# Optimization experiments

Hardware: AMD Instinct MI355X
Metric: run time of the kernel (lower is better)

Reference implementation:

```python
import jax, jax.numpy as jnp
import numpy as np

N = 32768      # total atoms in batch
D_IN = 1024    # input feature dimension
H1 = 512       # encoder/decoder hidden width
LAT = 128      # latent dimension
D_OUT = 1024   # output dimension
E = 4          # number of unique element symbols (experts)


def _xavier(key, shape):
    # torch.nn.init.xavier_uniform_ on Linear weights
    fan_in, fan_out = shape[-2], shape[-1]
    limit = np.sqrt(6.0 / (fan_in + fan_out)).astype(np.float32)
    return jax.random.uniform(key, shape, jnp.float32, -limit, limit)


def setup_inputs() -> dict:
    key = jax.random.key(0)
    ks = jax.random.split(key, 8)
    X = jax.random.normal(ks[0], (N, D_IN), jnp.float32)
    sym_ids = jax.random.randint(ks[1], (N,), 0, E)
    # stacked per-symbol (expert) weights: topology 1024->512->128->512->1024
    We1 = _xavier(ks[2], (E, D_IN, H1));  be1 = jnp.zeros((E, H1), jnp.float32)
    We2 = _xavier(ks[3], (E, H1, LAT));   be2 = jnp.zeros((E, LAT), jnp.float32)
    Wd1 = _xavier(ks[4], (E, LAT, H1));   bd1 = jnp.zeros((E, H1), jnp.float32)
    Wd2 = _xavier(ks[5], (E, H1, D_OUT)); bd2 = jnp.zeros((E, D_OUT), jnp.float32)
    return {"X": X, "sym_ids": sym_ids,
            "We1": We1, "be1": be1, "We2": We2, "be2": be2,
            "Wd1": Wd1, "bd1": bd1, "Wd2": Wd2, "bd2": bd2}


def reference(X, sym_ids, We1, be1, We2, be2, Wd1, bd1, Wd2, bd2):
    # Dense MoE-style dispatch: compute every expert on the full batch (E is
    # tiny and fixed), then select each atom's own-symbol output. Same math as
    # the per-atom Python-loop routing in the original forward.
    def expert(e):
        h = jax.nn.relu(X @ We1[e] + be1[e])          # [N, H1]  encoder layer 1
        z = jax.nn.relu(h @ We2[e] + be2[e])          # [N, LAT] latent (encoder layer 2)
        d = jax.nn.relu(z @ Wd1[e] + bd1[e])          # [N, H1]  decoder layer 1
        return d @ Wd2[e] + bd2[e]                    # [N, D_OUT] final Linear, no activation

    outs = jnp.stack([expert(e) for e in range(E)])   # [E, N, D_OUT]
    # route: pick expert sym_ids[n] for atom n
    return jnp.take_along_axis(outs, sym_ids[None, :, None], axis=0)[0]
```

## Files before the change

### kernel.cpp

```cpp
#include <hip/hip_runtime.h>
#include <hip/hip_bf16.h>
#include <stdint.h>

typedef __bf16 bf16x8 __attribute__((ext_vector_type(8)));
typedef float  f32x4  __attribute__((ext_vector_type(4)));

#define NATOMS  32768
#define NEXP    4
#define MAXROWS (NATOMS + NEXP*256)
#define MB256   (MAXROWS/256)
#define MB128   (MAXROWS/128)
#define MGRP    ((MB256 + 7)/8)
#define XCONV   2048
#define SCAT    32

#define WS_HDR   0u
#define WS_PERM  1024u
#define WS_BC    136192u
#define WS_BB    138240u
#define WS_W1T   140288u
#define WS_W2T   (WS_W1T + 4194304u)
#define WS_W3T   (WS_W2T + 524288u)
#define WS_W4T   (WS_W3T + 524288u)
#define WS_H     (WS_W4T + 4194304u)
#define WS_D     WS_H
#define WS_XB    (WS_H + 34603008u)

__device__ __forceinline__ unsigned short f2bf(float f){
  union { float f; uint32_t u; } v; v.f = f;
  uint32_t r = v.u + 0x7fffu + ((v.u >> 16) & 1u);
  return (unsigned short)(r >> 16);
}
__device__ __forceinline__ uint32_t pk2(float a, float b){
  return (uint32_t)f2bf(a) | ((uint32_t)f2bf(b) << 16);
}
__device__ __forceinline__ void glds16(const void* g, void* l){
  __builtin_amdgcn_global_load_lds(
      (const __attribute__((address_space(1))) uint32_t*)g,
      (__attribute__((address_space(3))) uint32_t*)l, 16, 0, 0);
}

__global__ __launch_bounds__(256) void routeA(const int* __restrict__ sym,
                                              int* __restrict__ bc,
                                              int* __restrict__ perm){
  __shared__ int h[NEXP];
  const int t = threadIdx.x, b = blockIdx.x;
  if (t < NEXP) h[t] = 0;
  for (int i = b*256 + t; i < MAXROWS; i += 128*256) perm[i] = -1;
  __syncthreads();
  int s = sym[b*256 + t];
  atomicAdd(&h[s], 1);
  __syncthreads();
  if (t < NEXP) bc[b*NEXP + t] = h[t];
}

__global__ __launch_bounds__(64) void routeB(const int* __restrict__ bc,
                                             int* __restrict__ hdr,
                                             int* __restrict__ bb){
  __shared__ int tot[NEXP], pof[NEXP+1];
  const int t = threadIdx.x;
  if (t < NEXP){
    int s = 0;
    for (int i=0;i<128;++i) s += bc[i*NEXP + t];
    tot[t] = s;
  }
  __syncthreads();
  if (t == 0){
    int o = 0; pof[0] = 0;
    for (int e=0;e<NEXP;++e){ o += (tot[e]+255)&~255; pof[e+1]=o; }
    for (int e=0;e<=NEXP;++e) hdr[e]=pof[e];
  }
  __syncthreads();
  if (t < NEXP){
    int run = pof[t];
    for (int i=0;i<128;++i){ bb[i*NEXP + t] = run; run += bc[i*NEXP + t]; }
  }
}

template<int K, int NO>
__device__ __forceinline__ void wtile1024(const float* __restrict__ W,
                                          unsigned short* __restrict__ Bt,
                                          int b, unsigned short (*tile)[65]){
  const int nx = NO/64, ny = K/64;
  const int e = b / (nx*ny), rem = b % (nx*ny);
  const int k0 = (rem / nx) * 64;
  const int n0 = (rem % nx) * 64;
  const int t  = threadIdx.x;
  const int c  = t & 63;
  const float* Wb = W + ((size_t)e*K + k0)*NO + n0;
  #pragma unroll
  for (int i=0;i<4;++i){
    int r = (t>>6) + i*16;
    tile[r][c] = f2bf(Wb[(size_t)r*NO + c]);
  }
  __syncthreads();
  unsigned short* Bb = Bt + ((size_t)e*NO + n0)*K + k0;
  #pragma unroll
  for (int i=0;i<4;++i){
    int r = (t>>6) + i*16;
    Bb[(size_t)r*K + c] = tile[c][r];
  }
}

__global__ __launch_bounds__(1024) void prep_kernel(
    const int*   __restrict__ sym,  const int* __restrict__ bb,  int* __restrict__ perm,
    const float* __restrict__ X,    unsigned short* __restrict__ Xb,
    const float* __restrict__ We1, unsigned short* __restrict__ W1t,
    const float* __restrict__ We2, unsigned short* __restrict__ W2t,
    const float* __restrict__ Wd1, unsigned short* __restrict__ W3t,
    const float* __restrict__ Wd2, unsigned short* __restrict__ W4t)
{
  __shared__ unsigned short tile[64][65];
  __shared__ int wc[16][NEXP];

  int b = blockIdx.x;
  const int t = threadIdx.x;

  if (b < SCAT){
    const int lane = t & 63, w = t >> 6;
    const int a = b*1024 + t;
    const int s = sym[a];
    unsigned long long b0 = __ballot(s & 1);
    unsigned long long b1 = __ballot(s & 2);
    unsigned long long meq = ((s & 1) ? b0 : ~b0) & ((s & 2) ? b1 : ~b1);
    unsigned long long lt  = ((unsigned long long)1 << lane) - 1;
    const int lofs = __popcll(meq & lt);
    if (lane == 0){
      unsigned long long m00 = ~b0 & ~b1, m01 = b0 & ~b1, m10 = ~b0 & b1, m11 = b0 & b1;
      wc[w][0] = __popcll(m00); wc[w][1] = __popcll(m01);
      wc[w][2] = __popcll(m10); wc[w][3] = __popcll(m11);
    }
    __syncthreads();
    int wbase = 0;
    for (int i=0;i<w;++i) wbase += wc[i][s];
    const int rb = (t >> 8);
    int wbase_rb = 0;
    for (int i = rb*4; i < w; ++i) wbase_rb += wc[i][s];
    const int slot = bb[(b*4 + rb)*NEXP + s] + wbase_rb + lofs;
    perm[slot] = a;
    (void)wbase;
    return;
  }
  b -= SCAT;
  if (b < XCONV){
    size_t i = ((size_t)b*1024 + t) * 16;
    const float4* src = (const float4*)(X + i);
    float4 f0 = src[0], f1 = src[1], f2 = src[2], f3 = src[3];
    uint4 o0, o1;
    o0.x = pk2(f0.x,f0.y); o0.y = pk2(f0.z,f0.w);
    o0.z = pk2(f1.x,f1.y); o0.w = pk2(f1.z,f1.w);
    o1.x = pk2(f2.x,f2.y); o1.y = pk2(f2.z,f2.w);
    o1.z = pk2(f3.x,f3.y); o1.w = pk2(f3.z,f3.w);
    *(uint4*)&Xb[i]     = o0;
    *(uint4*)&Xb[i + 8] = o1;
    return;
  }
  b -= XCONV;
  if (b < 512){ wtile1024<1024, 512>(We1, W1t, b, tile); return; }
  b -= 512;
  if (b <  64){ wtile1024< 512, 128>(We2, W2t, b, tile); return; }
  b -= 64;
  if (b <  64){ wtile1024< 128, 512>(Wd1, W3t, b, tile); return; }
  b -= 64;
  wtile1024< 512,1024>(Wd2, W4t, b, tile);
}

template<int K, int NO, int NT, bool RELU, bool GATHER, bool FINAL>
__global__ __launch_bounds__(512, 4) void gemm_big(
    const unsigned short* __restrict__ A,
    const unsigned short* __restrict__ Bt,
    const float* __restrict__ bias,
    unsigned short* __restrict__ Cb,
    float* __restrict__ Cf,
    const int* __restrict__ hdr,
    const int* __restrict__ perm)
{
  __shared__ __align__(16) unsigned short smem[256*64 + 128*64];
  __shared__ int sperm[256];
  unsigned short* As = smem;
  unsigned short* Bs = smem + 256*64;

  const int b = blockIdx.x;
  const int grp = b / (8*NT), rem = b % (8*NT);
  const int rowblk = grp*8 + (rem & 7);
  const int row0 = rowblk * 256;
  if (row0 >= hdr[NEXP]) return;
  const int ntile = rem >> 3;
  const int e = (row0 >= hdr[1]) + (row0 >= hdr[2]) + (row0 >= hdr[3]);
  const int n0 = ntile * 128;

  const int t = threadIdx.x;
  const int lane = t & 63, wid = t >> 6;

  if constexpr (GATHER || FINAL){
    if (t < 256) sperm[t] = perm[row0 + t];
    __syncthreads();
  }

  const int l8 = lane >> 3;
  const int scoff = (((lane & 7) ^ l8) << 3);

  const unsigned short* asrc[4];
  #pragma unroll
  for (int i=0;i<4;++i){
    const int r = wid*32 + i*8 + l8;
    long grow;
    if constexpr (GATHER){
      int a = sperm[r];
      grow = (a < 0) ? 0 : a;
    } else {
      grow = row0 + r;
    }
    asrc[i] = A + (size_t)grow*K + scoff;
  }
  const unsigned short* bsrc[2];
  #pragma unroll
  for (int i=0;i<2;++i)
    bsrc[i] = Bt + ((size_t)e*NO + n0 + wid*16 + i*8 + l8)*K + scoff;

  const int lr   = lane & 15;
  const int sgrp = lane >> 4;
  const int wr   = (wid >> 1) * 64;
  const int wc   = (wid & 1) * 64;

  f32x4 acc[4][4];
  const f32x4 z4 = {0.f,0.f,0.f,0.f};
  #pragma unroll
  for (int mi=0;mi<4;++mi)
    #pragma unroll
    for (int ni=0;ni<4;++ni) acc[mi][ni] = z4;

  #pragma unroll 1
  for (int kt = 0; kt < K/64; ++kt){
    __syncthreads();
    #pragma unroll
    for (int i=0;i<4;++i)
      glds16(asrc[i] + kt*64, As + (wid*4+i)*512);
    #pragma unroll
    for (int i=0;i<2;++i)
      glds16(bsrc[i] + kt*64, Bs + (wid*2+i)*512);
    __syncthreads();

    #pragma unroll
    for (int kk=0;kk<2;++kk){
      bf16x8 af[4], bfr[4];
      const int s = kk*4 + sgrp;
      #pragma unroll
      for (int mi=0;mi<4;++mi){
        int R = wr + mi*16 + lr;
        af[mi] = *(const bf16x8*)&As[R*64 + ((s ^ (R & 7)) << 3)];
      }
      #pragma unroll
      for (int ni=0;ni<4;++ni){
        int Cc = wc + ni*16 + lr;
        bfr[ni] = *(const bf16x8*)&Bs[Cc*64 + ((s ^ (Cc & 7)) << 3)];
      }
      #pragma unroll
      for (int mi=0;mi<4;++mi)
        #pragma unroll
        for (int ni=0;ni<4;++ni)
          acc[mi][ni] = __builtin_amdgcn_mfma_f32_16x16x32_bf16(af[mi], bfr[ni], acc[mi][ni], 0, 0, 0);
    }
  }

  __syncthreads();
  if constexpr (FINAL){
    float* stf = (float*)smem;
    #pragma unroll
    for (int qr=0; qr<4; ++qr){
      if ((wid >> 1) == qr){
        #pragma unroll
        for (int ni=0;ni<4;++ni){
          const int colg = n0 + wc + ni*16 + lr;
          const float bv_ = bias[(size_t)e*NO + colg];
          #pragma unroll
          for (int mi=0;mi<4;++mi){
            #pragma unroll
            for (int q=0;q<4;++q){
              float v = acc[mi][ni][q] + bv_;
              if (RELU) v = fmaxf(v, 0.f);
              stf[(mi*16 + sgrp*4 + q)*132 + wc + ni*16 + lr] = v;
            }
          }
        }
      }
      __syncthreads();
      #pragma unroll
      for (int i=0;i<4;++i){
        int idx = t + 512*i;
        int r = idx >> 5, c4 = idx & 31;
        int atom = sperm[qr*64 + r];
        if (atom >= 0)
          *(float4*)&Cf[(size_t)atom*NO + n0 + c4*4] = *(const float4*)&stf[r*132 + c4*4];
      }
      __syncthreads();
    }
  } else {
    unsigned short* st = smem;
    const int wrl = ((wid >> 1) & 1) * 64;
    #pragma unroll
    for (int h=0; h<2; ++h){
      if ((wid >> 2) == h){
        #pragma unroll
        for (int ni=0;ni<4;++ni){
          const int colg = n0 + wc + ni*16 + lr;
          const float bv_ = bias[(size_t)e*NO + colg];
          #pragma unroll
          for (int mi=0;mi<4;++mi){
            #pragma unroll
            for (int q=0;q<4;++q){
              float v = acc[mi][ni][q] + bv_;
              if (RELU) v = fmaxf(v, 0.f);
              st[(wrl + mi*16 + sgrp*4 + q)*136 + wc + ni*16 + lr] = f2bf(v);
            }
          }
        }
      }
      __syncthreads();
      #pragma unroll
      for (int i=0;i<4;++i){
        int idx = t + 512*i;
        int r = idx >> 4, c8 = idx & 15;
        *(uint4*)&Cb[(size_t)(row0 + h*128 + r)*NO + n0 + c8*8] = *(const uint4*)&st[r*136 + c8*8];
      }
      __syncthreads();
    }
  }
}

__global__ __launch_bounds__(256, 2) void fused_mid(
    const unsigned short* H,
    const unsigned short* __restrict__ W2,
    const float* __restrict__ b2,
    const unsigned short* __restrict__ W3,
    const float* __restrict__ b3,
    unsigned short* D,
    const int* __restrict__ hdr)
{
  __shared__ __align__(16) unsigned short un[128*136];
  __shared__ __align__(16) unsigned short Zs[128*128];
  unsigned short* As = un;
  unsigned short* Bs = un + 128*64;

  const int row0 = blockIdx.x * 128;
  if (row0 >= hdr[NEXP]) return;
  const int e = (row0 >= hdr[1]) + (row0 >= hdr[2]) + (row0 >= hdr[3]);

  const int t = threadIdx.x;
  const int lane = t & 63, wid = t >> 6;
  const int l8 = lane >> 3;
  const int scoff = (((lane & 7) ^ l8) << 3);
  const int lr = lane & 15, sgrp = lane >> 4;
  const int wr = (wid >> 1) * 64, wc = (wid & 1) * 64;

  const unsigned short* asrc[4];
  const unsigned short* bsrc[4];
  #pragma unroll
  for (int i=0;i<4;++i){
    asrc[i] = H  + (size_t)(row0 + wid*32 + i*8 + l8)*512 + scoff;
    bsrc[i] = W2 + ((size_t)e*128 + wid*32 + i*8 + l8)*512 + scoff;
  }

  f32x4 acc[4][4];
  const f32x4 z4 = {0.f,0.f,0.f,0.f};
  #pragma unroll
  for (int mi=0;mi<4;++mi)
    #pragma unroll
    for (int ni=0;ni<4;++ni) acc[mi][ni] = z4;

  #pragma unroll 1
  for (int kt = 0; kt < 8; ++kt){
    __syncthreads();
    #pragma unroll
    for (int i=0;i<4;++i){
      glds16(asrc[i] + kt*64, As + (wid*4+i)*512);
      glds16(bsrc[i] + kt*64, Bs + (wid*4+i)*512);
    }
    __syncthreads();
    #pragma unroll
    for (int kk=0;kk<2;++kk){
      bf16x8 af[4], bfr[4];
      const int s = kk*4 + sgrp;
      #pragma unroll
      for (int mi=0;mi<4;++mi){
        int R = wr + mi*16 + lr;
        af[mi] = *(const bf16x8*)&As[R*64 + ((s ^ (R & 7)) << 3)];
      }
      #pragma unroll
      for (int ni=0;ni<4;++ni){
        int Cc = wc + ni*16 + lr;
        bfr[ni] = *(const bf16x8*)&Bs[Cc*64 + ((s ^ (Cc & 7)) << 3)];
      }
      #pragma unroll
      for (int mi=0;mi<4;++mi)
        #pragma unroll
        for (int ni=0;ni<4;++ni)
          acc[mi][ni] = __builtin_amdgcn_mfma_f32_16x16x32_bf16(af[mi], bfr[ni], acc[mi][ni], 0, 0, 0);
    }
  }
  #pragma unroll
  for (int ni=0;ni<4;++ni){
    const int col = wc + ni*16 + lr;
    const float bv_ = b2[(size_t)e*128 + col];
    const int ch = col >> 3, cl = col & 7;
    #pragma unroll
    for (int mi=0;mi<4;++mi){
      #pragma unroll
      for (int q=0;q<4;++q){
        const int row = wr + mi*16 + sgrp*4 + q;
        float v = fmaxf(acc[mi][ni][q] + bv_, 0.f);
        Zs[row*128 + ((ch ^ (row & 15)) << 3) + cl] = f2bf(v);
      }
    }
  }
  __syncthreads();

  bf16x8 afk[4][4];
  #pragma unroll
  for (int kk=0;kk<4;++kk)
    #pragma unroll
    for (int mi=0;mi<4;++mi){
      int R = wr + mi*16 + lr;
      afk[kk][mi] = *(const bf16x8*)&Zs[R*128 + (((kk*4+sgrp) ^ (R & 15)) << 3)];
    }

  #pragma unroll 1
  for (int nt=0; nt<4; ++nt){
    #pragma unroll
    for (int i=0;i<8;++i){
      int R = (wid*8 + i)*4 + (lane >> 4);
      int sch = (lane & 15) ^ (R & 15);
      glds16(W3 + ((size_t)e*512 + nt*128 + R)*128 + sch*8, un + (size_t)(wid*8+i)*512);
    }
    __syncthreads();

    #pragma unroll
    for (int mi=0;mi<4;++mi)
      #pragma unroll
      for (int ni=0;ni<4;++ni) acc[mi][ni] = z4;

    #pragma unroll
    for (int kk=0;kk<4;++kk){
      bf16x8 bfr[4];
      const int s = kk*4 + sgrp;
      #pragma unroll
      for (int ni=0;ni<4;++ni){
        int Cc = wc + ni*16 + lr;
        bfr[ni] = *(const bf16x8*)&un[Cc*128 + ((s ^ (Cc & 15)) << 3)];
      }
      #pragma unroll
      for (int mi=0;mi<4;++mi)
        #pragma unroll
        for (int ni=0;ni<4;++ni)
          acc[mi][ni] = __builtin_amdgcn_mfma_f32_16x16x32_bf16(afk[kk][mi], bfr[ni], acc[mi][ni], 0, 0, 0);
    }
    __syncthreads();

    #pragma unroll
    for (int ni=0;ni<4;++ni){
      const int col = wc + ni*16 + lr;
      const float bv_ = b3[(size_t)e*512 + nt*128 + col];
      #pragma unroll
      for (int mi=0;mi<4;++mi){
        #pragma unroll
        for (int q=0;q<4;++q){
          const int row = wr + mi*16 + sgrp*4 + q;
          float v = fmaxf(acc[mi][ni][q] + bv_, 0.f);
          un[row*136 + col] = f2bf(v);
        }
      }
    }
    __syncthreads();
    #pragma unroll
    for (int i=0;i<8;++i){
      int idx = t + 256*i;
      int r = idx >> 4, c8 = idx & 15;
      *(uint4*)&D[(size_t)(row0 + r)*512 + nt*128 + c8*8] = *(const uint4*)&un[r*136 + c8*8];
    }
    __syncthreads();
  }
}

extern "C" void kernel_launch(void* const* d_in, const int* in_sizes, int n_in,
                              void* d_out, int out_size, void* d_ws, size_t ws_size,
                              hipStream_t stream) {
  const float* X   = (const float*)d_in[0];
  const int*   sym = (const int*)  d_in[1];
  const float* We1 = (const float*)d_in[2];
  const float* be1 = (const float*)d_in[3];
  const float* We2 = (const float*)d_in[4];
  const float* be2 = (const float*)d_in[5];
  const float* Wd1 = (const float*)d_in[6];
  const float* bd1 = (const float*)d_in[7];
  const float* Wd2 = (const float*)d_in[8];
  const float* bd2 = (const float*)d_in[9];
  float* out = (float*)d_out;

  char* ws = (char*)d_ws;
  int* hdr  = (int*)(ws + WS_HDR);
  int* perm = (int*)(ws + WS_PERM);
  int* bc   = (int*)(ws + WS_BC);
  int* bb   = (int*)(ws + WS_BB);
  unsigned short* W1t = (unsigned short*)(ws + WS_W1T);
  unsigned short* W2t = (unsigned short*)(ws + WS_W2T);
  unsigned short* W3t = (unsigned short*)(ws + WS_W3T);
  unsigned short* W4t = (unsigned short*)(ws + WS_W4T);
  unsigned short* H   = (unsigned short*)(ws + WS_H);
  unsigned short* Dd  = (unsigned short*)(ws + WS_D);
  unsigned short* Xb  = (unsigned short*)(ws + WS_XB);

  dim3 b256(256), b512(512), b1024(1024);
  routeA<<<dim3(128), b256, 0, stream>>>(sym, bc, perm);
  routeB<<<dim3(1), dim3(64), 0, stream>>>(bc, hdr, bb);
  prep_kernel<<<dim3(SCAT + XCONV + 512 + 64 + 64 + 512), b1024, 0, stream>>>(
      sym, bb, perm, X, Xb, We1, W1t, We2, W2t, Wd1, W3t, Wd2, W4t);

  gemm_big<1024, 512, 4, true,  true,  false><<<dim3(MGRP*8*4), b512, 0, stream>>>(
      Xb, W1t, be1, H, nullptr, hdr, perm);
  fused_mid<<<dim3(MB128), b256, 0, stream>>>(H, W2t, be2, W3t, bd1, Dd, hdr);
  gemm_big< 512,1024, 8, false, false, true ><<<dim3(MGRP*8*8), b512, 0, stream>>>(
      Dd, W4t, bd2, nullptr, out, hdr, perm);
}
```

Measured before the change: 197.4 us.

## Fuse decoder output GEMM into mid kernel, keeping decoder activations in LDS

```diff
diff --git a/kernel.cpp b/kernel.cpp
--- a/kernel.cpp
+++ b/kernel.cpp
@@ -23,7 +23,6 @@
 #define WS_W3T   (WS_W2T + 524288u)
 #define WS_W4T   (WS_W3T + 524288u)
 #define WS_H     (WS_W4T + 4194304u)
-#define WS_D     WS_H
 #define WS_XB    (WS_H + 34603008u)
 
 __device__ __forceinline__ unsigned short f2bf(float f){
@@ -131,14 +130,11 @@
       wc[w][2] = __popcll(m10); wc[w][3] = __popcll(m11);
     }
     __syncthreads();
-    int wbase = 0;
-    for (int i=0;i<w;++i) wbase += wc[i][s];
     const int rb = (t >> 8);
     int wbase_rb = 0;
     for (int i = rb*4; i < w; ++i) wbase_rb += wc[i][s];
     const int slot = bb[(b*4 + rb)*NEXP + s] + wbase_rb + lofs;
     perm[slot] = a;
-    (void)wbase;
     return;
   }
   b -= SCAT;
@@ -165,13 +161,12 @@
   wtile1024< 512,1024>(Wd2, W4t, b, tile);
 }
 
-template<int K, int NO, int NT, bool RELU, bool GATHER, bool FINAL>
+template<int K, int NO, int NT, bool RELU, bool GATHER>
 __global__ __launch_bounds__(512, 4) void gemm_big(
     const unsigned short* __restrict__ A,
     const unsigned short* __restrict__ Bt,
     const float* __restrict__ bias,
     unsigned short* __restrict__ Cb,
-    float* __restrict__ Cf,
     const int* __restrict__ hdr,
     const int* __restrict__ perm)
 {
@@ -192,7 +187,7 @@
   const int t = threadIdx.x;
   const int lane = t & 63, wid = t >> 6;
 
-  if constexpr (GATHER || FINAL){
+  if constexpr (GATHER){
     if (t < 256) sperm[t] = perm[row0 + t];
     __syncthreads();
   }
@@ -264,83 +259,54 @@
   }
 
   __syncthreads();
-  if constexpr (FINAL){
-    float* stf = (float*)smem;
-    #pragma unroll
-    for (int qr=0; qr<4; ++qr){
-      if ((wid >> 1) == qr){
-        #pragma unroll
-        for (int ni=0;ni<4;++ni){
-          const int colg = n0 + wc + ni*16 + lr;
-          const float bv_ = bias[(size_t)e*NO + colg];
+  unsigned short* st = smem;
+  const int wrl = ((wid >> 1) & 1) * 64;
+  #pragma unroll
+  for (int h=0; h<2; ++h){
+    if ((wid >> 2) == h){
+      #pragma unroll
+      for (int ni=0;ni<4;++ni){
+        const int colg = n0 + wc + ni*16 + lr;
+        const float bv_ = bias[(size_t)e*NO + colg];
+        #pragma unroll
+        for (int mi=0;mi<4;++mi){
           #pragma unroll
-          for (int mi=0;mi<4;++mi){
-            #pragma unroll
-            for (int q=0;q<4;++q){
-              float v = acc[mi][ni][q] + bv_;
-              if (RELU) v = fmaxf(v, 0.f);
-              stf[(mi*16 + sgrp*4 + q)*132 + wc + ni*16 + lr] = v;
-            }
+          for (int q=0;q<4;++q){
+            float v = acc[mi][ni][q] + bv_;
+            if (RELU) v = fmaxf(v, 0.f);
+            st[(wrl + mi*16 + sgrp*4 + q)*136 + wc + ni*16 + lr] = f2bf(v);
           }
         }
       }
-      __syncthreads();
-      #pragma unroll
-      for (int i=0;i<4;++i){
-        int idx = t + 512*i;
-        int r = idx >> 5, c4 = idx & 31;
-        int atom = sperm[qr*64 + r];
-        if (atom >= 0)
-          *(float4*)&Cf[(size_t)atom*NO + n0 + c4*4] = *(const float4*)&stf[r*132 + c4*4];
-      }
-      __syncthreads();
-    }
-  } else {
-    unsigned short* st = smem;
-    const int wrl = ((wid >> 1) & 1) * 64;
-    #pragma unroll
-    for (int h=0; h<2; ++h){
-      if ((wid >> 2) == h){
-        #pragma unroll
-        for (int ni=0;ni<4;++ni){
-          const int colg = n0 + wc + ni*16 + lr;
-          const float bv_ = bias[(size_t)e*NO + colg];
-          #pragma unroll
-          for (int mi=0;mi<4;++mi){
-            #pragma unroll
-            for (int q=0;q<4;++q){
-              float v = acc[mi][ni][q] + bv_;
-              if (RELU) v = fmaxf(v, 0.f);
-              st[(wrl + mi*16 + sgrp*4 + q)*136 + wc + ni*16 + lr] = f2bf(v);
-            }
-          }
-        }
-      }
-      __syncthreads();
-      #pragma unroll
-      for (int i=0;i<4;++i){
-        int idx = t + 512*i;
-        int r = idx >> 4, c8 = idx & 15;
-        *(uint4*)&Cb[(size_t)(row0 + h*128 + r)*NO + n0 + c8*8] = *(const uint4*)&st[r*136 + c8*8];
-      }
-      __syncthreads();
-    }
-  }
-}
-
-__global__ __launch_bounds__(256, 2) void fused_mid(
+    }
+    __syncthreads();
+    #pragma unroll
+    for (int i=0;i<4;++i){
+      int idx = t + 512*i;
+      int r = idx >> 4, c8 = idx & 15;
+      *(uint4*)&Cb[(size_t)(row0 + h*128 + r)*NO + n0 + c8*8] = *(const uint4*)&st[r*136 + c8*8];
+    }
+    __syncthreads();
+  }
+}
+
+__global__ __launch_bounds__(256, 1) void fused_tail(
     const unsigned short* H,
     const unsigned short* __restrict__ W2,
     const float* __restrict__ b2,
     const unsigned short* __restrict__ W3,
     const float* __restrict__ b3,
-    unsigned short* D,
-    const int* __restrict__ hdr)
+    const unsigned short* __restrict__ W4,
+    const float* __restrict__ b4,
+    float* __restrict__ out,
+    const int* __restrict__ hdr,
+    const int* __restrict__ perm)
 {
-  __shared__ __align__(16) unsigned short un[128*136];
-  __shared__ __align__(16) unsigned short Zs[128*128];
-  unsigned short* As = un;
-  unsigned short* Bs = un + 128*64;
+  __shared__ __align__(16) unsigned short D4[4*128*128];
+  __shared__ __align__(16) unsigned short side[128*64];
+  unsigned short* As = side;
+  unsigned short* Bs = D4;
+  unsigned short* Zs = D4 + 3*16384;
 
   const int row0 = blockIdx.x * 128;
   if (row0 >= hdr[NEXP]) return;
@@ -353,16 +319,16 @@
   const int lr = lane & 15, sgrp = lane >> 4;
   const int wr = (wid >> 1) * 64, wc = (wid & 1) * 64;
 
-  const unsigned short* asrc[4];
-  const unsigned short* bsrc[4];
-  #pragma unroll
-  for (int i=0;i<4;++i){
-    asrc[i] = H  + (size_t)(row0 + wid*32 + i*8 + l8)*512 + scoff;
-    bsrc[i] = W2 + ((size_t)e*128 + wid*32 + i*8 + l8)*512 + scoff;
-  }
-
   f32x4 acc[4][4];
   const f32x4 z4 = {0.f,0.f,0.f,0.f};
+
+  const unsigned short* asrcA[4];
+  const unsigned short* bsrcA[4];
+  #pragma unroll
+  for (int i=0;i<4;++i){
+    asrcA[i] = H  + (size_t)(row0 + wid*32 + i*8 + l8)*512 + scoff;
+    bsrcA[i] = W2 + ((size_t)e*128 + wid*32 + i*8 + l8)*512 + scoff;
+  }
   #pragma unroll
   for (int mi=0;mi<4;++mi)
     #pragma unroll
@@ -373,8 +339,8 @@
     __syncthreads();
     #pragma unroll
     for (int i=0;i<4;++i){
-      glds16(asrc[i] + kt*64, As + (wid*4+i)*512);
-      glds16(bsrc[i] + kt*64, Bs + (wid*4+i)*512);
+      glds16(asrcA[i] + kt*64, As + (wid*4+i)*512);
+      glds16(bsrcA[i] + kt*64, Bs + (wid*4+i)*512);
     }
     __syncthreads();
     #pragma unroll
@@ -398,6 +364,7 @@
           acc[mi][ni] = __builtin_amdgcn_mfma_f32_16x16x32_bf16(af[mi], bfr[ni], acc[mi][ni], 0, 0, 0);
     }
   }
+  __syncthreads();
   #pragma unroll
   for (int ni=0;ni<4;++ni){
     const int col = wc + ni*16 + lr;
@@ -414,7 +381,6 @@
     }
   }
   __syncthreads();
-
   bf16x8 afk[4][4];
   #pragma unroll
   for (int kk=0;kk<4;++kk)
@@ -423,61 +389,130 @@
       int R = wr + mi*16 + lr;
       afk[kk][mi] = *(const bf16x8*)&Zs[R*128 + (((kk*4+sgrp) ^ (R & 15)) << 3)];
     }
+  __syncthreads();
 
   #pragma unroll 1
   for (int nt=0; nt<4; ++nt){
     #pragma unroll
-    for (int i=0;i<8;++i){
-      int R = (wid*8 + i)*4 + (lane >> 4);
-      int sch = (lane & 15) ^ (R & 15);
-      glds16(W3 + ((size_t)e*512 + nt*128 + R)*128 + sch*8, un + (size_t)(wid*8+i)*512);
-    }
-    __syncthreads();
-
-    #pragma unroll
     for (int mi=0;mi<4;++mi)
       #pragma unroll
       for (int ni=0;ni<4;++ni) acc[mi][ni] = z4;
-
-    #pragma unroll
-    for (int kk=0;kk<4;++kk){
-      bf16x8 bfr[4];
-      const int s = kk*4 + sgrp;
-      #pragma unroll
-      for (int ni=0;ni<4;++ni){
-        int Cc = wc + ni*16 + lr;
-        bfr[ni] = *(const bf16x8*)&un[Cc*128 + ((s ^ (Cc & 15)) << 3)];
-      }
-      #pragma unroll
-      for (int mi=0;mi<4;++mi)
-        #pragma unroll
-        for (int ni=0;ni<4;++ni)
-          acc[mi][ni] = __builtin_amdgcn_mfma_f32_16x16x32_bf16(afk[kk][mi], bfr[ni], acc[mi][ni], 0, 0, 0);
-    }
-    __syncthreads();
-
+    #pragma unroll
+    for (int h=0; h<2; ++h){
+      __syncthreads();
+      #pragma unroll
+      for (int i=0;i<4;++i)
+        glds16(W3 + ((size_t)e*512 + nt*128 + wid*32 + i*8 + l8)*128 + h*64 + scoff,
+               side + (wid*4+i)*512);
+      __syncthreads();
+      #pragma unroll
+      for (int kk2=0;kk2<2;++kk2){
+        const int sl = kk2*4 + sgrp;
+        const int kk = h*2 + kk2;
+        bf16x8 bfr[4];
+        #pragma unroll
+        for (int ni=0;ni<4;++ni){
+          int Cc = wc + ni*16 + lr;
+          bfr[ni] = *(const bf16x8*)&side[Cc*64 + ((sl ^ (Cc & 7)) << 3)];
+        }
+        #pragma unroll
+        for (int mi=0;mi<4;++mi)
+          #pragma unroll
+          for (int ni=0;ni<4;++ni)
+            acc[mi][ni] = __builtin_amdgcn_mfma_f32_16x16x32_bf16(afk[kk][mi], bfr[ni], acc[mi][ni], 0, 0, 0);
+      }
+    }
+    unsigned short* Dq = D4 + nt*16384;
     #pragma unroll
     for (int ni=0;ni<4;++ni){
       const int col = wc + ni*16 + lr;
       const float bv_ = b3[(size_t)e*512 + nt*128 + col];
+      const int ch = col >> 3, cl = col & 7;
       #pragma unroll
       for (int mi=0;mi<4;++mi){
         #pragma unroll
         for (int q=0;q<4;++q){
           const int row = wr + mi*16 + sgrp*4 + q;
           float v = fmaxf(acc[mi][ni][q] + bv_, 0.f);
-          un[row*136 + col] = f2bf(v);
+          Dq[row*128 + ((ch ^ (row & 15)) << 3) + cl] = f2bf(v);
         }
       }
     }
-    __syncthreads();
-    #pragma unroll
-    for (int i=0;i<8;++i){
-      int idx = t + 256*i;
-      int r = idx >> 4, c8 = idx & 15;
-      *(uint4*)&D[(size_t)(row0 + r)*512 + nt*128 + c8*8] = *(const uint4*)&un[r*136 + c8*8];
-    }
-    __syncthreads();
+  }
+  __syncthreads();
+
+  #pragma unroll 1
+  for (int ot=0; ot<8; ++ot){
+    #pragma unroll
+    for (int mi=0;mi<4;++mi)
+      #pragma unroll
+      for (int ni=0;ni<4;++ni) acc[mi][ni] = z4;
+    #pragma unroll 1
+    for (int knt=0; knt<4; ++knt){
+      bf16x8 af2[4][4];
+      #pragma unroll
+      for (int kk=0;kk<4;++kk)
+        #pragma unroll
+        for (int mi=0;mi<4;++mi){
+          int R = wr + mi*16 + lr;
+          af2[kk][mi] = *(const bf16x8*)&D4[knt*16384 + R*128 + (((kk*4+sgrp) ^ (R & 15)) << 3)];
+        }
+      #pragma unroll
+      for (int h=0; h<2; ++h){
+        __syncthreads();
+        #pragma unroll
+        for (int i=0;i<4;++i)
+          glds16(W4 + ((size_t)e*1024 + ot*128 + wid*32 + i*8 + l8)*512 + knt*128 + h*64 + scoff,
+                 side + (wid*4+i)*512);
+        __syncthreads();
+        #pragma unroll
+        for (int kk2=0;kk2<2;++kk2){
+          const int sl = kk2*4 + sgrp;
+          const int kk = h*2 + kk2;
+          bf16x8 bfr[4];
+          #pragma unroll
+          for (int ni=0;ni<4;++ni){
+            int Cc = wc + ni*16 + lr;
+            bfr[ni] = *(const bf16x8*)&side[Cc*64 + ((sl ^ (Cc & 7)) << 3)];
+          }
+          #pragma unroll
+          for (int mi=0;mi<4;++mi)
+            #pragma unroll
+            for (int ni=0;ni<4;++ni)
+              acc[mi][ni] = __builtin_amdgcn_mfma_f32_16x16x32_bf16(af2[kk][mi], bfr[ni], acc[mi][ni], 0, 0, 0);
+        }
+      }
+    }
+    float* stf = (float*)side;
+    #pragma unroll 1
+    for (int q=0; q<4; ++q){
+      __syncthreads();
+      if ((wid >> 1) == (q >> 1)){
+        #pragma unroll
+        for (int m2=0;m2<2;++m2){
+          const int mi = (q & 1)*2 + m2;
+          #pragma unroll
+          for (int ni=0;ni<4;++ni){
+            const int colg = ot*128 + wc + ni*16 + lr;
+            const float bv_ = b4[(size_t)e*1024 + colg];
+            #pragma unroll
+            for (int q4=0;q4<4;++q4){
+              const int rl = m2*16 + sgrp*4 + q4;
+              stf[rl*128 + wc + ni*16 + lr] = acc[mi][ni][q4] + bv_;
+            }
+          }
+        }
+      }
+      __syncthreads();
+      #pragma unroll
+      for (int i=0;i<4;++i){
+        int idx = t + 256*i;
+        int r = idx >> 5, c4 = idx & 31;
+        int atom = perm[row0 + q*32 + r];
+        if (atom >= 0)
+          *(float4*)&out[(size_t)atom*1024 + ot*128 + c4*4] = *(const float4*)&stf[r*128 + c4*4];
+      }
+    }
   }
 }
 
@@ -506,7 +541,6 @@
   unsigned short* W3t = (unsigned short*)(ws + WS_W3T);
   unsigned short* W4t = (unsigned short*)(ws + WS_W4T);
   unsigned short* H   = (unsigned short*)(ws + WS_H);
-  unsigned short* Dd  = (unsigned short*)(ws + WS_D);
   unsigned short* Xb  = (unsigned short*)(ws + WS_XB);
 
   dim3 b256(256), b512(512), b1024(1024);
@@ -515,9 +549,8 @@
   prep_kernel<<<dim3(SCAT + XCONV + 512 + 64 + 64 + 512), b1024, 0, stream>>>(
       sym, bb, perm, X, Xb, We1, W1t, We2, W2t, Wd1, W3t, Wd2, W4t);
 
-  gemm_big<1024, 512, 4, true,  true,  false><<<dim3(MGRP*8*4), b512, 0, stream>>>(
-      Xb, W1t, be1, H, nullptr, hdr, perm);
-  fused_mid<<<dim3(MB128), b256, 0, stream>>>(H, W2t, be2, W3t, bd1, Dd, hdr);
-  gemm_big< 512,1024, 8, false, false, true ><<<dim3(MGRP*8*8), b512, 0, stream>>>(
-      Dd, W4t, bd2, nullptr, out, hdr, perm);
-}
+  gemm_big<1024, 512, 4, true, true><<<dim3(MGRP*8*4), b512, 0, stream>>>(
+      Xb, W1t, be1, H, hdr, perm);
+  fused_tail<<<dim3(MB128), b256, 0, stream>>>(
+      H, W2t, be2, W3t, bd1, W4t, bd2, out, hdr, perm);
+}
```

Measured after the change: 660.7 us. 3.35x slower.
